# Kernel optimization log

Hardware: AMD Instinct MI355X
Metric: run time of the kernel (lower is better)

## Reference

```python
import jax, jax.numpy as jnp
import numpy as np

N_NODES = 100000
N_EDGES = 1600000
F_IN = 256
F_HID = 128
F_LAT = 2
VOCAB = 100000
N_SAMP = 512
LEAKY_SLOPE = 0.2


def setup_inputs() -> dict:
    key = jax.random.key(0)
    ks = jax.random.split(key, 16)
    inp = {
        "X_concat": jax.random.normal(ks[0], (N_NODES, F_IN), dtype=jnp.float32),
        "input_x": jax.random.randint(ks[1], (N_NODES,), 0, VOCAB),
        "input_y": jax.random.randint(ks[2], (N_NODES,), 0, VOCAB),
        "edge_index": jax.random.randint(ks[3], (2, N_EDGES), 0, N_NODES),
        "sample_ids": jax.random.randint(ks[4], (N_SAMP,), 0, VOCAB),
        # GATConv gc1 params
        "W1": jax.random.normal(ks[5], (F_IN, F_HID), dtype=jnp.float32) * 0.05,
        "a1_src": jax.random.normal(ks[6], (F_HID,), dtype=jnp.float32) * 0.05,
        "a1_dst": jax.random.normal(ks[7], (F_HID,), dtype=jnp.float32) * 0.05,
        # GATConv gc2_mu params
        "W_mu": jax.random.normal(ks[8], (F_HID, F_LAT), dtype=jnp.float32) * 0.05,
        "amu_src": jax.random.normal(ks[9], (F_LAT,), dtype=jnp.float32) * 0.05,
        "amu_dst": jax.random.normal(ks[10], (F_LAT,), dtype=jnp.float32) * 0.05,
        # GATConv gc2_sig params (computed by module; exp(log_sig) is discarded by forward)
        "W_sig": jax.random.normal(ks[11], (F_HID, F_LAT), dtype=jnp.float32) * 0.05,
        "asig_src": jax.random.normal(ks[12], (F_LAT,), dtype=jnp.float32) * 0.05,
        "asig_dst": jax.random.normal(ks[13], (F_LAT,), dtype=jnp.float32) * 0.05,
        # sampled-softmax output table
        "ss_weight": jax.random.normal(ks[14], (VOCAB, F_LAT), dtype=jnp.float32) * 0.05,
        "ss_bias": jnp.zeros((VOCAB,), dtype=jnp.float32),
    }
    return inp


def gat_conv(x, W, a_src, a_dst, src, dst, n_nodes):
    """Sparse GAT layer: edge score = leaky_relu(a_src.h[src] + a_dst.h[dst]),
    per-destination-node softmax, scatter-aggregate alpha * h[src]."""
    h = x @ W                                  # [N, F']
    e_src = h @ a_src                          # [N]
    e_dst = h @ a_dst                          # [N]
    e = jax.nn.leaky_relu(e_src[src] + e_dst[dst], LEAKY_SLOPE)  # [E]
    # numerically stable segment softmax over incoming edges of each dst node
    e_max = jax.ops.segment_max(e, dst, num_segments=n_nodes)    # [N]
    e_max = jnp.where(jnp.isfinite(e_max), e_max, 0.0)
    ex = jnp.exp(e - e_max[dst])               # [E]
    denom = jax.ops.segment_sum(ex, dst, num_segments=n_nodes)   # [N]
    alpha = ex / jnp.maximum(denom[dst], 1e-16)                  # [E]
    out = jax.ops.segment_sum(alpha[:, None] * h[src], dst, num_segments=n_nodes)
    return out                                 # [N, F']


def reference(X_concat, input_x, input_y, edge_index, sample_ids,
              W1, a1_src, a1_dst, W_mu, amu_src, amu_dst,
              W_sig, asig_src, asig_dst, ss_weight, ss_bias):
    src, dst = edge_index[0], edge_index[1]
    n = X_concat.shape[0]
    # GATEncoder (eval mode: dropout is identity)
    h1 = jax.nn.relu(gat_conv(X_concat, W1, a1_src, a1_dst, src, dst, n))
    mu = gat_conv(h1, W_mu, amu_src, amu_dst, src, dst, n)       # output_vectors
    # gc2_sig branch exists in the module but its output is discarded by forward
    # Sampled softmax: true-class logit + logits against sampled negatives
    true_w = ss_weight[input_y]                                  # [N, L]
    true_logit = jnp.sum(mu * true_w, axis=-1) + ss_bias[input_y]  # [N]
    samp_logits = mu @ ss_weight[sample_ids].T + ss_bias[sample_ids]  # [N, S]
    logits = jnp.concatenate([true_logit[:, None], samp_logits], axis=1)  # [N, 1+S]
    return (logits, mu)
```

## Files before the change

### kernel.cpp

```cpp
#include <hip/hip_runtime.h>
#include <hip/hip_fp16.h>
#include <math.h>

#define N_NODES 100000
#define N_EDGES 1600000
#define F_IN 256
#define F_HID 128
#define F_LAT 2
#define VOCAB 100000
#define N_SAMP 512
#define SLOPE 0.2f

#define CHUNK 1024
#define NCHUNK ((N_NODES + CHUNK - 1) / CHUNK)

typedef __attribute__((ext_vector_type(8))) short bf16x8;
typedef __attribute__((ext_vector_type(4))) float f32x4;

__device__ __forceinline__ ushort f2bf_rne(float f) {
    uint u = __float_as_uint(f);
    return (ushort)((u + 0x7FFFu + ((u >> 16) & 1u)) >> 16);
}

__global__ void k_hist(const int* __restrict__ dst, int* __restrict__ deg) {
    int e0 = (blockIdx.x * blockDim.x + threadIdx.x) * 4;
    if (e0 >= N_EDGES) return;
    int4 d4 = *(const int4*)&dst[e0];
    atomicAdd(&deg[d4.x], 1);
    atomicAdd(&deg[d4.y], 1);
    atomicAdd(&deg[d4.z], 1);
    atomicAdd(&deg[d4.w], 1);
}

__global__ void k_chunksum(const int* __restrict__ deg, int* __restrict__ csum) {
    __shared__ int s[256];
    int b = blockIdx.x, t = threadIdx.x;
    int base = b * CHUNK, v = 0;
    for (int i = t; i < CHUNK; i += 256) {
        int idx = base + i;
        if (idx < N_NODES) v += deg[idx];
    }
    s[t] = v; __syncthreads();
    for (int d = 128; d > 0; d >>= 1) { if (t < d) s[t] += s[t + d]; __syncthreads(); }
    if (t == 0) csum[b] = s[0];
}

__global__ void k_scan98(int* __restrict__ csum) {
    __shared__ int s[128];
    int t = threadIdx.x;
    int v = (t < NCHUNK) ? csum[t] : 0;
    s[t] = v; __syncthreads();
    for (int d = 1; d < 128; d <<= 1) {
        int u = (t >= d) ? s[t - d] : 0;
        __syncthreads();
        s[t] += u;
        __syncthreads();
    }
    if (t < NCHUNK) csum[t] = s[t] - v;
}

__global__ void k_offsets(const int* __restrict__ deg, const int* __restrict__ csum,
                          int* __restrict__ off) {
    __shared__ int sd[CHUNK];
    __shared__ int ss[256];
    int b = blockIdx.x, t = threadIdx.x, base = b * CHUNK;
    for (int i = t; i < CHUNK; i += 256) {
        int idx = base + i;
        sd[i] = (idx < N_NODES) ? deg[idx] : 0;
    }
    __syncthreads();
    int l0 = sd[t * 4], l1 = sd[t * 4 + 1], l2 = sd[t * 4 + 2], l3 = sd[t * 4 + 3];
    int tsum = l0 + l1 + l2 + l3;
    ss[t] = tsum; __syncthreads();
    for (int d = 1; d < 256; d <<= 1) {
        int v = 0;
        if (t >= d) v = ss[t - d];
        __syncthreads();
        ss[t] += v;
        __syncthreads();
    }
    int excl = ss[t] - tsum + csum[b];
    int p0 = excl, p1 = p0 + l0, p2 = p1 + l1, p3 = p2 + l2;
    int idx = base + t * 4;
    if (idx     < N_NODES) off[idx]     = p0;
    if (idx + 1 < N_NODES) off[idx + 1] = p1;
    if (idx + 2 < N_NODES) off[idx + 2] = p2;
    if (idx + 3 < N_NODES) off[idx + 3] = p3;
}

__global__ void k_packw(const float* __restrict__ W,
                        ushort* __restrict__ Whi, ushort* __restrict__ Wlo,
                        const int* __restrict__ sample_ids, const float* __restrict__ ssw,
                        const float* __restrict__ ssb, float4* __restrict__ stab) {
    if (blockIdx.x == 128) {
        for (int i = threadIdx.x; i < N_SAMP; i += 256) {
            int sid = sample_ids[i];
            stab[i] = make_float4(ssw[sid * 2], ssw[sid * 2 + 1], ssb[sid], 0.f);
        }
        return;
    }
    int t = blockIdx.x * 256 + threadIdx.x;
    int k = t >> 7, j = t & 127;
    float w = W[t];
    ushort h = f2bf_rne(w);
    float hf = __uint_as_float((uint)h << 16);
    ushort l = f2bf_rne(w - hf);
    int s = k >> 5, g = (k >> 3) & 3, e = k & 7, n = j >> 4;
    int lane = (j & 15) + 16 * g;
    int addr = ((s * 8 + n) * 64 + lane) * 8 + e;
    Whi[addr] = h; Wlo[addr] = l;
}

#define TBM 128
__launch_bounds__(256)
__global__ void k_gemm1m(const float* __restrict__ X,
                         const ushort* __restrict__ Whi, const ushort* __restrict__ Wlo,
                         const float* __restrict__ a_src, const float* __restrict__ a_dst,
                         __half* __restrict__ h, float* __restrict__ es, float* __restrict__ ed) {
    __shared__ ushort Ah[2][8][64][8];
    __shared__ ushort Al[2][8][64][8];
    __shared__ float esp[TBM][2];
    __shared__ float edp[TBM][2];

    int tid = threadIdx.x;
    int lane = tid & 63;
    int wid = tid >> 6;
    int wm = wid >> 1;
    int wn = wid & 1;
    int l15 = lane & 15, lg = lane >> 4;
    int row0 = blockIdx.x * TBM;

    f32x4 acc[4][4];
#pragma unroll
    for (int m = 0; m < 4; m++)
#pragma unroll
        for (int n = 0; n < 4; n++) acc[m][n] = (f32x4){0.f, 0.f, 0.f, 0.f};

    for (int kb = 0; kb < 4; kb++) {
#pragma unroll
        for (int i = 0; i < 8; i++) {
            int idx = tid + i * 256;
            int r = (idx & 15) | ((idx >> 8) << 4);
            int k4 = ((idx >> 4) & 15) << 2;
            int grow = row0 + r;
            float4 v = make_float4(0.f, 0.f, 0.f, 0.f);
            if (grow < N_NODES) v = *(const float4*)&X[(size_t)grow * F_IN + kb * 64 + k4];
            uint u0 = __float_as_uint(v.x), u1 = __float_as_uint(v.y);
            uint u2 = __float_as_uint(v.z), u3 = __float_as_uint(v.w);
            ushort h0 = (ushort)(u0 >> 16), h1 = (ushort)(u1 >> 16);
            ushort h2 = (ushort)(u2 >> 16), h3 = (ushort)(u3 >> 16);
            float r0 = v.x - __uint_as_float(u0 & 0xFFFF0000u);
            float r1 = v.y - __uint_as_float(u1 & 0xFFFF0000u);
            float r2 = v.z - __uint_as_float(u2 & 0xFFFF0000u);
            float r3 = v.w - __uint_as_float(u3 & 0xFFFF0000u);
            ushort l0 = (ushort)(__float_as_uint(r0) >> 16);
            ushort l1 = (ushort)(__float_as_uint(r1) >> 16);
            ushort l2 = (ushort)(__float_as_uint(r2) >> 16);
            ushort l3 = (ushort)(__float_as_uint(r3) >> 16);
            int s = k4 >> 5, g = (k4 >> 3) & 3, e = k4 & 7, m = r >> 4;
            int lsl = (r & 15) + 16 * g;
            *(ushort4*)&Ah[s][m][lsl][e] = make_ushort4(h0, h1, h2, h3);
            *(ushort4*)&Al[s][m][lsl][e] = make_ushort4(l0, l1, l2, l3);
        }
        __syncthreads();
#pragma unroll
        for (int s = 0; s < 2; s++) {
            int ks = kb * 2 + s;
            bf16x8 bh[4], bl[4];
#pragma unroll
            for (int n = 0; n < 4; n++) {
                size_t ba = (size_t)((ks * 8 + wn * 4 + n) * 64 + lane) * 8;
                bh[n] = *(const bf16x8*)(Whi + ba);
                bl[n] = *(const bf16x8*)(Wlo + ba);
            }
#pragma unroll
            for (int m = 0; m < 4; m++) {
                bf16x8 ah = *(const bf16x8*)&Ah[s][wm * 4 + m][lane][0];
                bf16x8 al = *(const bf16x8*)&Al[s][wm * 4 + m][lane][0];
#pragma unroll
                for (int n = 0; n < 4; n++) {
                    acc[m][n] = __builtin_amdgcn_mfma_f32_16x16x32_bf16(ah, bh[n], acc[m][n], 0, 0, 0);
                    acc[m][n] = __builtin_amdgcn_mfma_f32_16x16x32_bf16(ah, bl[n], acc[m][n], 0, 0, 0);
                    acc[m][n] = __builtin_amdgcn_mfma_f32_16x16x32_bf16(al, bh[n], acc[m][n], 0, 0, 0);
                }
            }
        }
        __syncthreads();
    }

    float asv[4], adv[4];
#pragma unroll
    for (int n = 0; n < 4; n++) {
        asv[n] = a_src[wn * 64 + n * 16 + l15];
        adv[n] = a_dst[wn * 64 + n * 16 + l15];
    }
#pragma unroll
    for (int m = 0; m < 4; m++) {
#pragma unroll
        for (int j = 0; j < 4; j++) {
            int row = wm * 64 + m * 16 + lg * 4 + j;
            int grow = row0 + row;
            if (grow < N_NODES) {
                __half* hp = h + (size_t)grow * F_HID + wn * 64 + l15;
#pragma unroll
                for (int n = 0; n < 4; n++) hp[n * 16] = __float2half_rn(acc[m][n][j]);
            }
            float sv = 0.f, dv = 0.f;
#pragma unroll
            for (int n = 0; n < 4; n++) {
                sv = fmaf(acc[m][n][j], asv[n], sv);
                dv = fmaf(acc[m][n][j], adv[n], dv);
            }
#pragma unroll
            for (int o = 8; o; o >>= 1) { sv += __shfl_xor(sv, o, 16); dv += __shfl_xor(dv, o, 16); }
            if (l15 == 0) { esp[row][wn] = sv; edp[row][wn] = dv; }
        }
    }
    __syncthreads();
    if (tid < TBM) {
        int grow = row0 + tid;
        if (grow < N_NODES) {
            es[grow] = esp[tid][0] + esp[tid][1];
            ed[grow] = edp[tid][0] + edp[tid][1];
        }
    }
}

__global__ void k_scatter(const int* __restrict__ src, const int* __restrict__ dst,
                          const float* __restrict__ es, const float* __restrict__ ed,
                          const int* __restrict__ off, int* __restrict__ cursor,
                          int2* __restrict__ epack) {
    int e0 = (blockIdx.x * blockDim.x + threadIdx.x) * 4;
    if (e0 >= N_EDGES) return;
    int4 s4 = *(const int4*)&src[e0];
    int4 d4 = *(const int4*)&dst[e0];
    float x0 = es[s4.x] + ed[d4.x];
    float x1 = es[s4.y] + ed[d4.y];
    float x2 = es[s4.z] + ed[d4.z];
    float x3 = es[s4.w] + ed[d4.w];
    x0 = (x0 >= 0.f) ? x0 : SLOPE * x0;
    x1 = (x1 >= 0.f) ? x1 : SLOPE * x1;
    x2 = (x2 >= 0.f) ? x2 : SLOPE * x2;
    x3 = (x3 >= 0.f) ? x3 : SLOPE * x3;
    int p0 = off[d4.x] + atomicAdd(&cursor[d4.x], 1);
    int p1 = off[d4.y] + atomicAdd(&cursor[d4.y], 1);
    int p2 = off[d4.z] + atomicAdd(&cursor[d4.z], 1);
    int p3 = off[d4.w] + atomicAdd(&cursor[d4.w], 1);
    epack[p0] = make_int2(s4.x, __float_as_int(x0));
    epack[p1] = make_int2(s4.y, __float_as_int(x1));
    epack[p2] = make_int2(s4.z, __float_as_int(x2));
    epack[p3] = make_int2(s4.w, __float_as_int(x3));
}

__global__ void k_agg1(const __half* __restrict__ h, const int* __restrict__ off,
                       const int* __restrict__ deg, const int2* __restrict__ epack,
                       const float* __restrict__ W_mu,
                       const float* __restrict__ amu_src, const float* __restrict__ amu_dst,
                       float4* __restrict__ n4) {
    int node = blockIdx.x * 4 + (threadIdx.x >> 6);
    int lane = threadIdx.x & 63;
    if (node >= N_NODES) return;
    int start = off[node], n = deg[node];
    const int2* pp = epack + start;
    int half = lane >> 5, sl = lane & 31;
    const __half* hb = h + 4 * sl;

    float a0 = 0.f, a1 = 0.f, a2 = 0.f, a3 = 0.f, ssum = 0.f;
    int i = half;
    for (; i + 6 < n; i += 8) {
        int2 p0 = pp[i], p1 = pp[i + 2], p2 = pp[i + 4], p3 = pp[i + 6];
        float w0 = __expf(__int_as_float(p0.y));
        float w1 = __expf(__int_as_float(p1.y));
        float w2 = __expf(__int_as_float(p2.y));
        float w3 = __expf(__int_as_float(p3.y));
        ushort4 u0 = *(const ushort4*)(hb + (size_t)p0.x * F_HID);
        ushort4 u1 = *(const ushort4*)(hb + (size_t)p1.x * F_HID);
        ushort4 u2 = *(const ushort4*)(hb + (size_t)p2.x * F_HID);
        ushort4 u3 = *(const ushort4*)(hb + (size_t)p3.x * F_HID);
        ssum += (w0 + w1) + (w2 + w3);
        float2 rA, rB;
        rA = __half22float2(*(const __half2*)&u0.x); rB = __half22float2(*(const __half2*)&u0.z);
        a0 = fmaf(w0, rA.x, a0); a1 = fmaf(w0, rA.y, a1); a2 = fmaf(w0, rB.x, a2); a3 = fmaf(w0, rB.y, a3);
        rA = __half22float2(*(const __half2*)&u1.x); rB = __half22float2(*(const __half2*)&u1.z);
        a0 = fmaf(w1, rA.x, a0); a1 = fmaf(w1, rA.y, a1); a2 = fmaf(w1, rB.x, a2); a3 = fmaf(w1, rB.y, a3);
        rA = __half22float2(*(const __half2*)&u2.x); rB = __half22float2(*(const __half2*)&u2.z);
        a0 = fmaf(w2, rA.x, a0); a1 = fmaf(w2, rA.y, a1); a2 = fmaf(w2, rB.x, a2); a3 = fmaf(w2, rB.y, a3);
        rA = __half22float2(*(const __half2*)&u3.x); rB = __half22float2(*(const __half2*)&u3.z);
        a0 = fmaf(w3, rA.x, a0); a1 = fmaf(w3, rA.y, a1); a2 = fmaf(w3, rB.x, a2); a3 = fmaf(w3, rB.y, a3);
    }
    for (; i < n; i += 2) {
        int2 p = pp[i];
        float w = __expf(__int_as_float(p.y));
        ushort4 u = *(const ushort4*)(hb + (size_t)p.x * F_HID);
        float2 rA = __half22float2(*(const __half2*)&u.x);
        float2 rB = __half22float2(*(const __half2*)&u.z);
        ssum += w;
        a0 = fmaf(w, rA.x, a0); a1 = fmaf(w, rA.y, a1); a2 = fmaf(w, rB.x, a2); a3 = fmaf(w, rB.y, a3);
    }
    a0 += __shfl_xor(a0, 32); a1 += __shfl_xor(a1, 32);
    a2 += __shfl_xor(a2, 32); a3 += __shfl_xor(a3, 32);
    ssum += __shfl_xor(ssum, 32);

    float inv = 1.f / fmaxf(ssum, 1e-16f);
    float h0 = fmaxf(a0 * inv, 0.f), h1v = fmaxf(a1 * inv, 0.f);
    float h2 = fmaxf(a2 * inv, 0.f), h3v = fmaxf(a3 * inv, 0.f);

    float4 wA = *(const float4*)&W_mu[8 * sl];
    float4 wB = *(const float4*)&W_mu[8 * sl + 4];
    float q0 = h0 * wA.x + h1v * wA.z + h2 * wB.x + h3v * wB.z;
    float q1 = h0 * wA.y + h1v * wA.w + h2 * wB.y + h3v * wB.w;
#pragma unroll
    for (int o = 16; o; o >>= 1) { q0 += __shfl_down(q0, o); q1 += __shfl_down(q1, o); }
    if (lane == 0) {
        float4 v;
        v.x = q0;
        v.y = q1;
        v.z = q0 * amu_src[0] + q1 * amu_src[1];
        v.w = q0 * amu_dst[0] + q1 * amu_dst[1];
        n4[node] = v;
    }
}

__global__ void k_agg2(const float4* __restrict__ n4, const int* __restrict__ off,
                       const int* __restrict__ deg, const int2* __restrict__ epack,
                       float* __restrict__ mu_out) {
    int node = blockIdx.x * (blockDim.x >> 4) + (threadIdx.x >> 4);
    int lane = threadIdx.x & 15;
    if (node >= N_NODES) return;
    int start = off[node], n = deg[node];
    const int2* pp = epack + start;
    float edn = n4[node].w;
    float s = 0.f, a0 = 0.f, a1 = 0.f;
    for (int i = lane; i < n; i += 16) {
        float4 v = n4[pp[i].x];
        float x = v.z + edn;
        x = (x >= 0.f) ? x : SLOPE * x;
        float w = __expf(x);
        s += w;
        a0 = fmaf(w, v.x, a0);
        a1 = fmaf(w, v.y, a1);
    }
#pragma unroll
    for (int o = 8; o; o >>= 1) {
        s  += __shfl_xor(s, o, 16);
        a0 += __shfl_xor(a0, o, 16);
        a1 += __shfl_xor(a1, o, 16);
    }
    if (lane == 0) {
        float inv = 1.f / fmaxf(s, 1e-16f);
        float2 v = {a0 * inv, a1 * inv};
        *(float2*)(mu_out + node * 2) = v;
    }
}

__global__ void k_logits(const float* __restrict__ mu, const int* __restrict__ input_y,
                         const float4* __restrict__ stab, const float* __restrict__ ssw,
                         const float* __restrict__ ssb, float* __restrict__ out) {
    __shared__ float4 st[N_SAMP];
    __shared__ float tl[16];
    __shared__ float2 mus[16];
    int t = threadIdx.x;
    int nb = blockIdx.x * 16;
    for (int i = t; i < N_SAMP; i += 256) st[i] = stab[i];
    if (t < 16) {
        int node = nb + t;
        float2 mv = *(const float2*)&mu[node * 2];
        mus[t] = mv;
        int y = input_y[node];
        tl[t] = mv.x * ssw[y * 2] + mv.y * ssw[y * 2 + 1] + ssb[y];
    }
    __syncthreads();
#pragma unroll 1
    for (int k = 0; k < 16; k++) {
        int node = nb + k;
        float2 mv = mus[k];
        float* orow = out + (size_t)node * (N_SAMP + 1);
        for (int j = t; j < N_SAMP + 1; j += 256) {
            float v;
            if (j == 0) {
                v = tl[k];
            } else {
                float4 sv = st[j - 1];
                v = mv.x * sv.x + mv.y * sv.y + sv.z;
            }
            orow[j] = v;
        }
    }
}

extern "C" void kernel_launch(void* const* d_in, const int* in_sizes, int n_in,
                              void* d_out, int out_size, void* d_ws, size_t ws_size,
                              hipStream_t stream) {
    const float* X          = (const float*)d_in[0];
    const int*   input_y    = (const int*)d_in[2];
    const int*   edge_index = (const int*)d_in[3];
    const int*   sample_ids = (const int*)d_in[4];
    const float* W1         = (const float*)d_in[5];
    const float* a1_src     = (const float*)d_in[6];
    const float* a1_dst     = (const float*)d_in[7];
    const float* W_mu       = (const float*)d_in[8];
    const float* amu_src    = (const float*)d_in[9];
    const float* amu_dst    = (const float*)d_in[10];
    const float* ssw        = (const float*)d_in[14];
    const float* ssb        = (const float*)d_in[15];
    const int* src = edge_index;
    const int* dst = edge_index + N_EDGES;
    float* out = (float*)d_out;

    char* ws = (char*)d_ws;
    size_t o = 0;
    __half* h       = (__half*)(ws + o); o += (size_t)N_NODES * F_HID * 2;
    float* es       = (float*)(ws + o); o += (size_t)N_NODES * 4;
    float* ed       = (float*)(ws + o); o += (size_t)N_NODES * 4;
    float4* n4      = (float4*)(ws + o); o += (size_t)N_NODES * 16;
    int*   deg      = (int*)(ws + o);   o += (size_t)N_NODES * 4;
    int*   cursor   = (int*)(ws + o);   o += (size_t)N_NODES * 4;
    int*   off      = (int*)(ws + o);   o += (size_t)N_NODES * 4;
    int*   csum     = (int*)(ws + o);   o += 128 * 4;
    float4* stab    = (float4*)(ws + o); o += (size_t)N_SAMP * 16;
    int2*  epack    = (int2*)(ws + o);  o += (size_t)N_EDGES * 8;
    float* mu = out + (size_t)N_NODES * (N_SAMP + 1);

    ushort* whi = (ushort*)n4;
    ushort* wlo = whi + (size_t)8 * 8 * 64 * 8;

    hipMemsetAsync(deg, 0, (size_t)2 * N_NODES * 4, stream);

    const int E4B = (N_EDGES / 4 + 255) / 256;

    k_hist<<<E4B, 256, 0, stream>>>(dst, deg);
    k_chunksum<<<NCHUNK, 256, 0, stream>>>(deg, csum);
    k_scan98<<<1, 128, 0, stream>>>(csum);
    k_offsets<<<NCHUNK, 256, 0, stream>>>(deg, csum, off);

    k_packw<<<129, 256, 0, stream>>>(W1, whi, wlo, sample_ids, ssw, ssb, stab);
    k_gemm1m<<<(N_NODES + TBM - 1) / TBM, 256, 0, stream>>>(X, whi, wlo, a1_src, a1_dst, h, es, ed);
    k_scatter<<<E4B, 256, 0, stream>>>(src, dst, es, ed, off, cursor, epack);
    k_agg1<<<N_NODES / 4, 256, 0, stream>>>(h, off, deg, epack, W_mu, amu_src, amu_dst, n4);

    k_agg2<<<(N_NODES * 16 + 255) / 256, 256, 0, stream>>>(n4, off, deg, epack, mu);

    k_logits<<<N_NODES / 16, 256, 0, stream>>>(mu, input_y, stab, ssw, ssb, out);
}
```

Baseline: 615.5 us.

## Record atomic ranks in histogram, scatter source-only CSR, compute edge scores in aggregation

The histogram kernel now stores each edge's atomic rank, so the scatter kernel places source indices without a second atomic pass and without the cursor array. The scatter only writes 4-byte source ids and no longer depends on the GEMM outputs. Edge scores are instead recomputed inside agg1 from es/ed. agg1 also switches to 16 lanes × 8 halves per row with 4 edge slots, giving wider loads and more edges in flight. In exchange there is an extra rank array write and read, plus random es gathers in agg1.

```diff
diff --git a/kernel.cpp b/kernel.cpp
--- a/kernel.cpp
+++ b/kernel.cpp
@@ -22,14 +22,16 @@
     return (ushort)((u + 0x7FFFu + ((u >> 16) & 1u)) >> 16);
 }
 
-__global__ void k_hist(const int* __restrict__ dst, int* __restrict__ deg) {
+__global__ void k_hist(const int* __restrict__ dst, int* __restrict__ deg,
+                       int* __restrict__ rank) {
     int e0 = (blockIdx.x * blockDim.x + threadIdx.x) * 4;
     if (e0 >= N_EDGES) return;
     int4 d4 = *(const int4*)&dst[e0];
-    atomicAdd(&deg[d4.x], 1);
-    atomicAdd(&deg[d4.y], 1);
-    atomicAdd(&deg[d4.z], 1);
-    atomicAdd(&deg[d4.w], 1);
+    int r0 = atomicAdd(&deg[d4.x], 1);
+    int r1 = atomicAdd(&deg[d4.y], 1);
+    int r2 = atomicAdd(&deg[d4.z], 1);
+    int r3 = atomicAdd(&deg[d4.w], 1);
+    *(int4*)&rank[e0] = make_int4(r0, r1, r2, r3);
 }
 
 __global__ void k_chunksum(const int* __restrict__ deg, int* __restrict__ csum) {
@@ -227,33 +229,22 @@
 }
 
 __global__ void k_scatter(const int* __restrict__ src, const int* __restrict__ dst,
-                          const float* __restrict__ es, const float* __restrict__ ed,
-                          const int* __restrict__ off, int* __restrict__ cursor,
-                          int2* __restrict__ epack) {
+                          const int* __restrict__ rank, const int* __restrict__ off,
+                          int* __restrict__ srcs) {
     int e0 = (blockIdx.x * blockDim.x + threadIdx.x) * 4;
     if (e0 >= N_EDGES) return;
     int4 s4 = *(const int4*)&src[e0];
     int4 d4 = *(const int4*)&dst[e0];
-    float x0 = es[s4.x] + ed[d4.x];
-    float x1 = es[s4.y] + ed[d4.y];
-    float x2 = es[s4.z] + ed[d4.z];
-    float x3 = es[s4.w] + ed[d4.w];
-    x0 = (x0 >= 0.f) ? x0 : SLOPE * x0;
-    x1 = (x1 >= 0.f) ? x1 : SLOPE * x1;
-    x2 = (x2 >= 0.f) ? x2 : SLOPE * x2;
-    x3 = (x3 >= 0.f) ? x3 : SLOPE * x3;
-    int p0 = off[d4.x] + atomicAdd(&cursor[d4.x], 1);
-    int p1 = off[d4.y] + atomicAdd(&cursor[d4.y], 1);
-    int p2 = off[d4.z] + atomicAdd(&cursor[d4.z], 1);
-    int p3 = off[d4.w] + atomicAdd(&cursor[d4.w], 1);
-    epack[p0] = make_int2(s4.x, __float_as_int(x0));
-    epack[p1] = make_int2(s4.y, __float_as_int(x1));
-    epack[p2] = make_int2(s4.z, __float_as_int(x2));
-    epack[p3] = make_int2(s4.w, __float_as_int(x3));
+    int4 r4 = *(const int4*)&rank[e0];
+    srcs[off[d4.x] + r4.x] = s4.x;
+    srcs[off[d4.y] + r4.y] = s4.y;
+    srcs[off[d4.z] + r4.z] = s4.z;
+    srcs[off[d4.w] + r4.w] = s4.w;
 }
 
 __global__ void k_agg1(const __half* __restrict__ h, const int* __restrict__ off,
-                       const int* __restrict__ deg, const int2* __restrict__ epack,
+                       const int* __restrict__ deg, const int* __restrict__ srcs,
+                       const float* __restrict__ es, const float* __restrict__ ed,
                        const float* __restrict__ W_mu,
                        const float* __restrict__ amu_src, const float* __restrict__ amu_dst,
                        float4* __restrict__ n4) {
@@ -261,56 +252,69 @@
     int lane = threadIdx.x & 63;
     if (node >= N_NODES) return;
     int start = off[node], n = deg[node];
-    const int2* pp = epack + start;
-    int half = lane >> 5, sl = lane & 31;
-    const __half* hb = h + 4 * sl;
-
-    float a0 = 0.f, a1 = 0.f, a2 = 0.f, a3 = 0.f, ssum = 0.f;
-    int i = half;
-    for (; i + 6 < n; i += 8) {
-        int2 p0 = pp[i], p1 = pp[i + 2], p2 = pp[i + 4], p3 = pp[i + 6];
-        float w0 = __expf(__int_as_float(p0.y));
-        float w1 = __expf(__int_as_float(p1.y));
-        float w2 = __expf(__int_as_float(p2.y));
-        float w3 = __expf(__int_as_float(p3.y));
-        ushort4 u0 = *(const ushort4*)(hb + (size_t)p0.x * F_HID);
-        ushort4 u1 = *(const ushort4*)(hb + (size_t)p1.x * F_HID);
-        ushort4 u2 = *(const ushort4*)(hb + (size_t)p2.x * F_HID);
-        ushort4 u3 = *(const ushort4*)(hb + (size_t)p3.x * F_HID);
-        ssum += (w0 + w1) + (w2 + w3);
-        float2 rA, rB;
-        rA = __half22float2(*(const __half2*)&u0.x); rB = __half22float2(*(const __half2*)&u0.z);
-        a0 = fmaf(w0, rA.x, a0); a1 = fmaf(w0, rA.y, a1); a2 = fmaf(w0, rB.x, a2); a3 = fmaf(w0, rB.y, a3);
-        rA = __half22float2(*(const __half2*)&u1.x); rB = __half22float2(*(const __half2*)&u1.z);
-        a0 = fmaf(w1, rA.x, a0); a1 = fmaf(w1, rA.y, a1); a2 = fmaf(w1, rB.x, a2); a3 = fmaf(w1, rB.y, a3);
-        rA = __half22float2(*(const __half2*)&u2.x); rB = __half22float2(*(const __half2*)&u2.z);
-        a0 = fmaf(w2, rA.x, a0); a1 = fmaf(w2, rA.y, a1); a2 = fmaf(w2, rB.x, a2); a3 = fmaf(w2, rB.y, a3);
-        rA = __half22float2(*(const __half2*)&u3.x); rB = __half22float2(*(const __half2*)&u3.z);
-        a0 = fmaf(w3, rA.x, a0); a1 = fmaf(w3, rA.y, a1); a2 = fmaf(w3, rB.x, a2); a3 = fmaf(w3, rB.y, a3);
-    }
-    for (; i < n; i += 2) {
-        int2 p = pp[i];
-        float w = __expf(__int_as_float(p.y));
-        ushort4 u = *(const ushort4*)(hb + (size_t)p.x * F_HID);
-        float2 rA = __half22float2(*(const __half2*)&u.x);
-        float2 rB = __half22float2(*(const __half2*)&u.z);
+    const int* sp = srcs + start;
+    int slot = lane >> 4, l16 = lane & 15;
+    float edn = ed[node];
+    const __half* hb = h + 8 * l16;
+
+    float a0 = 0.f, a1 = 0.f, a2 = 0.f, a3 = 0.f;
+    float a4 = 0.f, a5 = 0.f, a6 = 0.f, a7 = 0.f, ssum = 0.f;
+    int i = slot;
+    for (; i + 4 < n; i += 8) {
+        int sA = sp[i], sB = sp[i + 4];
+        float xA = es[sA] + edn, xB = es[sB] + edn;
+        xA = (xA >= 0.f) ? xA : SLOPE * xA;
+        xB = (xB >= 0.f) ? xB : SLOPE * xB;
+        float wA = __expf(xA), wB = __expf(xB);
+        uint4 uA = *(const uint4*)(hb + (size_t)sA * F_HID);
+        uint4 uB = *(const uint4*)(hb + (size_t)sB * F_HID);
+        ssum += wA + wB;
+        float2 f0, f1, f2, f3;
+        f0 = __half22float2(*(const __half2*)&uA.x); f1 = __half22float2(*(const __half2*)&uA.y);
+        f2 = __half22float2(*(const __half2*)&uA.z); f3 = __half22float2(*(const __half2*)&uA.w);
+        a0 = fmaf(wA, f0.x, a0); a1 = fmaf(wA, f0.y, a1); a2 = fmaf(wA, f1.x, a2); a3 = fmaf(wA, f1.y, a3);
+        a4 = fmaf(wA, f2.x, a4); a5 = fmaf(wA, f2.y, a5); a6 = fmaf(wA, f3.x, a6); a7 = fmaf(wA, f3.y, a7);
+        f0 = __half22float2(*(const __half2*)&uB.x); f1 = __half22float2(*(const __half2*)&uB.y);
+        f2 = __half22float2(*(const __half2*)&uB.z); f3 = __half22float2(*(const __half2*)&uB.w);
+        a0 = fmaf(wB, f0.x, a0); a1 = fmaf(wB, f0.y, a1); a2 = fmaf(wB, f1.x, a2); a3 = fmaf(wB, f1.y, a3);
+        a4 = fmaf(wB, f2.x, a4); a5 = fmaf(wB, f2.y, a5); a6 = fmaf(wB, f3.x, a6); a7 = fmaf(wB, f3.y, a7);
+    }
+    for (; i < n; i += 4) {
+        int s = sp[i];
+        float x = es[s] + edn;
+        x = (x >= 0.f) ? x : SLOPE * x;
+        float w = __expf(x);
+        uint4 u = *(const uint4*)(hb + (size_t)s * F_HID);
         ssum += w;
-        a0 = fmaf(w, rA.x, a0); a1 = fmaf(w, rA.y, a1); a2 = fmaf(w, rB.x, a2); a3 = fmaf(w, rB.y, a3);
-    }
-    a0 += __shfl_xor(a0, 32); a1 += __shfl_xor(a1, 32);
-    a2 += __shfl_xor(a2, 32); a3 += __shfl_xor(a3, 32);
-    ssum += __shfl_xor(ssum, 32);
-
+        float2 f0 = __half22float2(*(const __half2*)&u.x), f1 = __half22float2(*(const __half2*)&u.y);
+        float2 f2 = __half22float2(*(const __half2*)&u.z), f3 = __half22float2(*(const __half2*)&u.w);
+        a0 = fmaf(w, f0.x, a0); a1 = fmaf(w, f0.y, a1); a2 = fmaf(w, f1.x, a2); a3 = fmaf(w, f1.y, a3);
+        a4 = fmaf(w, f2.x, a4); a5 = fmaf(w, f2.y, a5); a6 = fmaf(w, f3.x, a6); a7 = fmaf(w, f3.y, a7);
+    }
+#pragma unroll
+    for (int o = 16; o <= 32; o <<= 1) {
+        a0 += __shfl_xor(a0, o); a1 += __shfl_xor(a1, o);
+        a2 += __shfl_xor(a2, o); a3 += __shfl_xor(a3, o);
+        a4 += __shfl_xor(a4, o); a5 += __shfl_xor(a5, o);
+        a6 += __shfl_xor(a6, o); a7 += __shfl_xor(a7, o);
+        ssum += __shfl_xor(ssum, o);
+    }
     float inv = 1.f / fmaxf(ssum, 1e-16f);
     float h0 = fmaxf(a0 * inv, 0.f), h1v = fmaxf(a1 * inv, 0.f);
     float h2 = fmaxf(a2 * inv, 0.f), h3v = fmaxf(a3 * inv, 0.f);
-
-    float4 wA = *(const float4*)&W_mu[8 * sl];
-    float4 wB = *(const float4*)&W_mu[8 * sl + 4];
-    float q0 = h0 * wA.x + h1v * wA.z + h2 * wB.x + h3v * wB.z;
-    float q1 = h0 * wA.y + h1v * wA.w + h2 * wB.y + h3v * wB.w;
-#pragma unroll
-    for (int o = 16; o; o >>= 1) { q0 += __shfl_down(q0, o); q1 += __shfl_down(q1, o); }
+    float h4 = fmaxf(a4 * inv, 0.f), h5v = fmaxf(a5 * inv, 0.f);
+    float h6 = fmaxf(a6 * inv, 0.f), h7v = fmaxf(a7 * inv, 0.f);
+
+    float4 w0 = *(const float4*)&W_mu[16 * l16];
+    float4 w1 = *(const float4*)&W_mu[16 * l16 + 4];
+    float4 w2 = *(const float4*)&W_mu[16 * l16 + 8];
+    float4 w3 = *(const float4*)&W_mu[16 * l16 + 12];
+    float q0 = h0 * w0.x + h1v * w0.z + h2 * w1.x + h3v * w1.z
+             + h4 * w2.x + h5v * w2.z + h6 * w3.x + h7v * w3.z;
+    float q1 = h0 * w0.y + h1v * w0.w + h2 * w1.y + h3v * w1.w
+             + h4 * w2.y + h5v * w2.w + h6 * w3.y + h7v * w3.w;
+#pragma unroll
+    for (int o = 8; o; o >>= 1) { q0 += __shfl_down(q0, o, 16); q1 += __shfl_down(q1, o, 16); }
     if (lane == 0) {
         float4 v;
         v.x = q0;
@@ -322,17 +326,17 @@
 }
 
 __global__ void k_agg2(const float4* __restrict__ n4, const int* __restrict__ off,
-                       const int* __restrict__ deg, const int2* __restrict__ epack,
+                       const int* __restrict__ deg, const int* __restrict__ srcs,
                        float* __restrict__ mu_out) {
     int node = blockIdx.x * (blockDim.x >> 4) + (threadIdx.x >> 4);
     int lane = threadIdx.x & 15;
     if (node >= N_NODES) return;
     int start = off[node], n = deg[node];
-    const int2* pp = epack + start;
+    const int* sp = srcs + start;
     float edn = n4[node].w;
     float s = 0.f, a0 = 0.f, a1 = 0.f;
     for (int i = lane; i < n; i += 16) {
-        float4 v = n4[pp[i].x];
+        float4 v = n4[sp[i]];
         float x = v.z + edn;
         x = (x >= 0.f) ? x : SLOPE * x;
         float w = __expf(x);
@@ -414,31 +418,31 @@
     float* ed       = (float*)(ws + o); o += (size_t)N_NODES * 4;
     float4* n4      = (float4*)(ws + o); o += (size_t)N_NODES * 16;
     int*   deg      = (int*)(ws + o);   o += (size_t)N_NODES * 4;
-    int*   cursor   = (int*)(ws + o);   o += (size_t)N_NODES * 4;
     int*   off      = (int*)(ws + o);   o += (size_t)N_NODES * 4;
     int*   csum     = (int*)(ws + o);   o += 128 * 4;
     float4* stab    = (float4*)(ws + o); o += (size_t)N_SAMP * 16;
-    int2*  epack    = (int2*)(ws + o);  o += (size_t)N_EDGES * 8;
+    int*   rank     = (int*)(ws + o);   o += (size_t)N_EDGES * 4;
+    int*   srcs     = (int*)(ws + o);   o += (size_t)N_EDGES * 4;
     float* mu = out + (size_t)N_NODES * (N_SAMP + 1);
 
     ushort* whi = (ushort*)n4;
     ushort* wlo = whi + (size_t)8 * 8 * 64 * 8;
 
-    hipMemsetAsync(deg, 0, (size_t)2 * N_NODES * 4, stream);
+    hipMemsetAsync(deg, 0, (size_t)N_NODES * 4, stream);
 
     const int E4B = (N_EDGES / 4 + 255) / 256;
 
-    k_hist<<<E4B, 256, 0, stream>>>(dst, deg);
+    k_hist<<<E4B, 256, 0, stream>>>(dst, deg, rank);
     k_chunksum<<<NCHUNK, 256, 0, stream>>>(deg, csum);
     k_scan98<<<1, 128, 0, stream>>>(csum);
     k_offsets<<<NCHUNK, 256, 0, stream>>>(deg, csum, off);
+    k_scatter<<<E4B, 256, 0, stream>>>(src, dst, rank, off, srcs);
 
     k_packw<<<129, 256, 0, stream>>>(W1, whi, wlo, sample_ids, ssw, ssb, stab);
     k_gemm1m<<<(N_NODES + TBM - 1) / TBM, 256, 0, stream>>>(X, whi, wlo, a1_src, a1_dst, h, es, ed);
-    k_scatter<<<E4B, 256, 0, stream>>>(src, dst, es, ed, off, cursor, epack);
-    k_agg1<<<N_NODES / 4, 256, 0, stream>>>(h, off, deg, epack, W_mu, amu_src, amu_dst, n4);
-
-    k_agg2<<<(N_NODES * 16 + 255) / 256, 256, 0, stream>>>(n4, off, deg, epack, mu);
+    k_agg1<<<N_NODES / 4, 256, 0, stream>>>(h, off, deg, srcs, es, ed, W_mu, amu_src, amu_dst, n4);
+
+    k_agg2<<<(N_NODES * 16 + 255) / 256, 256, 0, stream>>>(n4, off, deg, srcs, mu);
 
     k_logits<<<N_NODES / 16, 256, 0, stream>>>(mu, input_y, stab, ssw, ssb, out);
 }
```

Measured after the change: 564.8 us. -8.2%, faster.
